# Kernel tuning notes

Measured on AMD Instinct MI355X. Metric: run time of the kernel, lower is better.

The kernel has to match this reference:

```python
import jax, jax.numpy as jnp
import numpy as np

DIM, H, KV, HD = 2048, 32, 8, 64
NREP = H // KV
EPS = 1e-6
NEG = -1e30


def _rope(x, cos, sin):
    # x: [B,S,h,HD], cos/sin: [S,HD//2]
    xr, xi = x[..., 0::2], x[..., 1::2]
    c = cos[None, :, None, :]
    s = sin[None, :, None, :]
    out = jnp.stack([xr * c - xi * s, xr * s + xi * c], axis=-1)
    return out.reshape(x.shape)


def _rmsnorm(x, w):
    xf = x.astype(jnp.float32)
    inv = jax.lax.rsqrt(jnp.mean(xf * xf, axis=-1, keepdims=True) + EPS)
    return (xf * inv * w).astype(x.dtype)


def setup_inputs() -> dict:
    key = jax.random.key(0)
    ks = jax.random.split(key, 9)
    B, S = 1, 2048
    x = jax.random.normal(ks[0], (B, S, DIM), jnp.float32)
    cos = jax.random.uniform(ks[1], (S, HD // 2), jnp.float32)
    sin = jax.random.uniform(ks[2], (S, HD // 2), jnp.float32)
    sc = 1.0 / np.sqrt(DIM)
    wq = jax.random.normal(ks[3], (DIM, DIM), jnp.float32) * sc
    wk = jax.random.normal(ks[4], (KV * HD, DIM), jnp.float32) * sc
    wv = jax.random.normal(ks[5], (KV * HD, DIM), jnp.float32) * sc
    wo = jax.random.normal(ks[6], (DIM, DIM), jnp.float32) * sc
    wg = jax.random.normal(ks[7], (DIM, DIM), jnp.float32) * sc
    qn = jnp.ones((HD,), jnp.float32)
    kn = jnp.ones((HD,), jnp.float32)
    return {"x": x, "cos": cos, "sin": sin, "wq": wq, "wk": wk, "wv": wv,
            "wo": wo, "wg": wg, "qn": qn, "kn": kn}


def reference(x, cos, sin, wq, wk, wv, wo, wg, qn, kn):
    B, S, _ = x.shape
    q = (x @ wq.T).reshape(B, S, H, HD)
    k = (x @ wk.T).reshape(B, S, KV, HD)
    v = (x @ wv.T).reshape(B, S, KV, HD)
    q = _rope(q, cos, sin)
    k = _rope(k, cos, sin)
    q = _rmsnorm(q, qn)
    k = _rmsnorm(k, kn)
    # GQA without materializing repeat_kv: head h = g*NREP + r uses kv head g
    qg = q.reshape(B, S, KV, NREP, HD)
    scale = 1.0 / np.sqrt(HD)
    scores = jnp.einsum('bqgrd,bkgd->bgrqk', qg, k) * scale  # [B,KV,NREP,S,S]
    causal = jnp.tril(jnp.ones((S, S), bool))
    scores = jnp.where(causal, scores, NEG)
    attn = jax.nn.softmax(scores, axis=-1)
    o = jnp.einsum('bgrqk,bkgd->bqgrd', attn, v).reshape(B, S, DIM)
    o = o * jax.nn.sigmoid(x @ wg.T)
    return o @ wo.T
```

## Files before the change

kernel.cpp:

```cpp
#include <hip/hip_runtime.h>
#include <stdint.h>

typedef unsigned short u16;
typedef __bf16 bf16x8 __attribute__((ext_vector_type(8)));
typedef float f32x4 __attribute__((ext_vector_type(4)));

__device__ __forceinline__ float bf2f(u16 u) {
  union { unsigned int i; float f; } v; v.i = ((unsigned int)u) << 16; return v.f;
}
__device__ __forceinline__ u16 f2bf(float f) {
  union { float f; unsigned int i; } v; v.f = f;
  unsigned int r = v.i + 0x7fffu + ((v.i >> 16) & 1u);
  return (u16)(r >> 16);
}
__device__ __forceinline__ u16 f2bf_trunc(float f) {
  union { float f; unsigned int i; } v; v.f = f;
  return (u16)(v.i >> 16);
}
__device__ __forceinline__ void ld16(const void* g, void* l) {
  __builtin_amdgcn_global_load_lds(
      (const __attribute__((address_space(1))) unsigned int*)g,
      (__attribute__((address_space(3))) unsigned int*)l, 16, 0, 0);
}

__global__ __launch_bounds__(256) void k_cast(
    const float* __restrict__ s0, u16* __restrict__ d0,
    const float* __restrict__ s1, u16* __restrict__ d1,
    const float* __restrict__ s2, u16* __restrict__ d2,
    const float* __restrict__ s3, u16* __restrict__ d3,
    const float* __restrict__ s4, u16* __restrict__ d4,
    const float* __restrict__ s5, u16* __restrict__ d5)
{
  int b = blockIdx.x;
  const float* s; u16* d;
  if (b < 4096)       { s = s0; d = d0; }
  else if (b < 8192)  { s = s1; d = d1; b -= 4096; }
  else if (b < 9216)  { s = s2; d = d2; b -= 8192; }
  else if (b < 10240) { s = s3; d = d3; b -= 9216; }
  else if (b < 14336) { s = s4; d = d4; b -= 10240; }
  else                { s = s5; d = d5; b -= 14336; }
  const int i = (b * 256 + threadIdx.x) * 4;
  const float4 v = *(const float4*)(s + i);
  ushort4 o;
  o.x = f2bf(v.x); o.y = f2bf(v.y); o.z = f2bf(v.z); o.w = f2bf(v.w);
  *(ushort4*)(d + i) = o;
}

template <typename OT>
__device__ __forceinline__ void gemm_body(
    const u16* __restrict__ A, int lda,
    const u16* __restrict__ B, int ldb,
    OT* __restrict__ C, int ldc, int K,
    u16* As, u16* Bs)
{
  const int tid = threadIdx.x;
  const int wave = tid >> 6, lane = tid & 63;
  const int wrow = (wave >> 1) * 64, wcol = (wave & 1) * 64;
  const int fr = lane & 15, kg = lane >> 4;
  const int srl = lane >> 3;
  const int scg = (lane & 7) ^ srl;

  f32x4 acc[4][4];
  const f32x4 z = {0.f, 0.f, 0.f, 0.f};
  for (int i = 0; i < 4; i++) for (int j = 0; j < 4; j++) acc[i][j] = z;

  const u16* Ag = A + (size_t)(wave * 8 + srl) * lda + scg * 8;
  const u16* Bg = B + (size_t)(wave * 8 + srl) * ldb + scg * 8;
  u16* Asw = As + wave * 8 * 64;
  u16* Bsw = Bs + wave * 8 * 64;
  const int sxr = fr & 7;

  for (int k0 = 0; k0 < K; k0 += 64) {
    for (int i = 0; i < 4; i++) {
      ld16(Ag + k0 + (size_t)(i * 32) * lda, Asw + i * 32 * 64);
      ld16(Bg + k0 + (size_t)(i * 32) * ldb, Bsw + i * 32 * 64);
    }
    __syncthreads();
    bf16x8 af[4][2], bfr[4][2];
    for (int i = 0; i < 4; i++)
      for (int h = 0; h < 2; h++) {
        af[i][h]  = *(const bf16x8*)&As[(wrow + i * 16 + fr) * 64 + (((h * 4 + kg) ^ sxr)) * 8];
        bfr[i][h] = *(const bf16x8*)&Bs[(wcol + i * 16 + fr) * 64 + (((h * 4 + kg) ^ sxr)) * 8];
      }
    for (int h = 0; h < 2; h++)
      for (int mi = 0; mi < 4; mi++)
        for (int ni = 0; ni < 4; ni++)
          acc[mi][ni] = __builtin_amdgcn_mfma_f32_16x16x32_bf16(af[mi][h], bfr[ni][h], acc[mi][ni], 0, 0, 0);
    __syncthreads();
  }
  const int er = kg * 4, ec = fr;
  for (int mi = 0; mi < 4; mi++)
    for (int ni = 0; ni < 4; ni++)
      for (int r = 0; r < 4; r++) {
        const float v = acc[mi][ni][r];
        OT* p = C + (size_t)(wrow + mi * 16 + er + r) * ldc + wcol + ni * 16 + ec;
        if constexpr (sizeof(OT) == 2) *p = (OT)f2bf(v); else *p = (OT)v;
      }
}

__global__ __launch_bounds__(256) void k_gemm_qkvg(
    const u16* __restrict__ x, const u16* __restrict__ wq, const u16* __restrict__ wk,
    const u16* __restrict__ wv, const u16* __restrict__ wg, u16* __restrict__ out)
{
  __shared__ __align__(16) u16 As[128 * 64];
  __shared__ __align__(16) u16 Bs[128 * 64];
  const int m0 = blockIdx.x * 128;
  const int c0 = blockIdx.y * 128;
  const u16* B; int br;
  if (c0 < 2048)      { B = wq; br = c0; }
  else if (c0 < 2560) { B = wk; br = c0 - 2048; }
  else if (c0 < 3072) { B = wv; br = c0 - 2560; }
  else                { B = wg; br = c0 - 3072; }
  gemm_body<u16>(x + (size_t)m0 * 2048, 2048, B + (size_t)br * 2048, 2048,
                 out + (size_t)m0 * 5120 + c0, 5120, 2048, As, Bs);
}

__global__ __launch_bounds__(256) void k_gemm_out(
    const u16* __restrict__ a, const u16* __restrict__ wo, float* __restrict__ out)
{
  __shared__ __align__(16) u16 As[128 * 64];
  __shared__ __align__(16) u16 Bs[128 * 64];
  const int m0 = blockIdx.x * 128;
  const int c0 = blockIdx.y * 128;
  gemm_body<float>(a + (size_t)m0 * 2048, 2048, wo + (size_t)c0 * 2048, 2048,
                   out + (size_t)m0 * 2048 + c0, 2048, 2048, As, Bs);
}

__global__ __launch_bounds__(256) void k_prep(
    u16* __restrict__ qkvg, const float* __restrict__ cosp, const float* __restrict__ sinp,
    const float* __restrict__ qn, const float* __restrict__ kn, u16* __restrict__ vt)
{
  __shared__ u16 Ls[64 * 72];
  if (blockIdx.x < 10240) {
    const int wid = (blockIdx.x * 256 + threadIdx.x) >> 6;
    const int lane = threadIdx.x & 63;
    const int s = wid / 20, hp = wid - s * 20;
    const int h = hp * 2 + (lane >> 5);
    const int j = lane & 31;
    u16* base; const float* wn;
    if (h < 32) { base = qkvg + (size_t)s * 5120 + h * 64;                wn = qn; }
    else        { base = qkvg + (size_t)s * 5120 + 2048 + (h - 32) * 64; wn = kn; }
    const unsigned int u = *(const unsigned int*)(base + 2 * j);
    const float xr = bf2f((u16)(u & 0xffffu)), xi = bf2f((u16)(u >> 16));
    const float c = cosp[s * 32 + j], sn = sinp[s * 32 + j];
    const float o0 = xr * c - xi * sn;
    const float o1 = xr * sn + xi * c;
    float ss = o0 * o0 + o1 * o1;
    for (int m = 1; m <= 16; m <<= 1) ss += __shfl_xor(ss, m, 64);
    const float inv = rsqrtf(ss * (1.0f / 64.0f) + 1e-6f);
    const u16 r0 = f2bf(o0 * inv * wn[2 * j]);
    const u16 r1 = f2bf(o1 * inv * wn[2 * j + 1]);
    *(unsigned int*)(base + 2 * j) = (unsigned int)r0 | ((unsigned int)r1 << 16);
  } else {
    const int bb = blockIdx.x - 10240;
    const int s0 = (bb & 31) * 64, g0 = (bb >> 5) * 64;
    const int tid = threadIdx.x;
    const int lr = tid >> 4, lc = (tid & 15) * 4;
    for (int p = 0; p < 4; p++) {
      const int r = p * 16 + lr;
      *(ushort4*)&Ls[r * 72 + lc] = *(const ushort4*)&qkvg[(size_t)(s0 + r) * 5120 + 2560 + g0 + lc];
    }
    __syncthreads();
    for (int p = 0; p < 4; p++) {
      const int r = p * 16 + lr;
      ushort4 o;
      o.x = Ls[(lc + 0) * 72 + r];
      o.y = Ls[(lc + 1) * 72 + r];
      o.z = Ls[(lc + 2) * 72 + r];
      o.w = Ls[(lc + 3) * 72 + r];
      *(ushort4*)&vt[(size_t)(g0 + r) * 2048 + s0 + lc] = o;
    }
  }
}

__global__ __launch_bounds__(256) void k_attn_part(
    const u16* __restrict__ qkvg, const u16* __restrict__ vt,
    u16* __restrict__ part, float* __restrict__ ml)
{
  __shared__ __align__(16) u16 Ks[128 * 64];
  __shared__ __align__(16) u16 Vs[64 * 128];
  __shared__ __align__(16) u16 Ps[64 * 132];
  const int c = blockIdx.x, h = blockIdx.y, g = h >> 2;
  int qt, ci;
  if (c < 8)       { qt = c;                 ci = 0; }
  else if (c < 24) { qt = 8 + ((c - 8) >> 1);  ci = (c - 8) & 1; }
  else if (c < 48) { qt = 16 + (c - 24) / 3;   ci = (c - 24) % 3; }
  else             { qt = 24 + ((c - 48) >> 2); ci = (c - 48) & 3; }
  const int kb0 = ci * 512;
  const int kend = min(kb0 + 512, (qt + 1) * 64);
  const int q0 = qt * 64;
  const int tid = threadIdx.x, wave = tid >> 6, lane = tid & 63;
  const int fr = lane & 15, kg = lane >> 4, fq = kg * 8;
  const int sx = fr & 7;

  {
    const u16* Qg = qkvg + (size_t)(q0 + wave * 16 + (lane >> 3)) * 5120 + h * 64 + (lane & 7) * 8;
    ld16(Qg, Ks + wave * 1024);
    ld16(Qg + (size_t)8 * 5120, Ks + wave * 1024 + 512);
  }
  __syncthreads();
  const bf16x8 aq0 = *(const bf16x8*)&Ks[(wave * 16 + fr) * 64 + fq];
  const bf16x8 aq1 = *(const bf16x8*)&Ks[(wave * 16 + fr) * 64 + 32 + fq];
  __syncthreads();

  f32x4 o[4];
  const f32x4 z = {0.f, 0.f, 0.f, 0.f};
  for (int i = 0; i < 4; i++) o[i] = z;
  float lsum[4] = {0.f, 0.f, 0.f, 0.f};
  const int qrow = q0 + wave * 16 + kg * 4;

  const int krl = wave * 8 + (lane >> 3);
  const int kcg = (lane & 7) ^ (krl & 7);
  const int vrl = wave * 4 + kg;
  const int vcg = fr ^ (vrl & 7);

  for (int kb = kb0; kb < kend; kb += 128) {
    {
      const u16* Kg = qkvg + (size_t)(kb + krl) * 5120 + 2048 + g * 64 + kcg * 8;
      for (int i = 0; i < 4; i++)
        ld16(Kg + (size_t)(i * 32) * 5120, Ks + (i * 32 + wave * 8) * 64);
    }
    {
      const u16* Vg = vt + (size_t)(g * 64 + vrl) * 2048 + kb + vcg * 8;
      for (int i = 0; i < 4; i++)
        ld16(Vg + (size_t)(i * 16) * 2048, Vs + (i * 16 + wave * 4) * 128);
    }
    __syncthreads();

    f32x4 sc[8];
    for (int i = 0; i < 8; i++) sc[i] = z;
    for (int ni = 0; ni < 8; ni++) {
      const bf16x8 bk0 = *(const bf16x8*)&Ks[(ni * 16 + fr) * 64 + (kg ^ sx) * 8];
      const bf16x8 bk1 = *(const bf16x8*)&Ks[(ni * 16 + fr) * 64 + ((kg + 4) ^ sx) * 8];
      sc[ni] = __builtin_amdgcn_mfma_f32_16x16x32_bf16(aq0, bk0, sc[ni], 0, 0, 0);
      sc[ni] = __builtin_amdgcn_mfma_f32_16x16x32_bf16(aq1, bk1, sc[ni], 0, 0, 0);
    }

    for (int r = 0; r < 4; r++) {
      float ls = 0.f;
      for (int ni = 0; ni < 8; ni++) {
        const int key = kb + ni * 16 + fr;
        float p = __expf(fmaf(sc[ni][r], 0.125f, -8.0f));
        p = (key <= qrow + r) ? p : 0.f;
        ls += p;
        Ps[(wave * 16 + kg * 4 + r) * 132 + ni * 16 + fr] = f2bf_trunc(p);
      }
      lsum[r] += ls;
    }

    for (int k0 = 0; k0 < 128; k0 += 32) {
      const bf16x8 ap = *(const bf16x8*)&Ps[(wave * 16 + fr) * 132 + k0 + fq];
      for (int ni = 0; ni < 4; ni++) {
        const bf16x8 bv = *(const bf16x8*)&Vs[(ni * 16 + fr) * 128 + (((k0 >> 3) + kg) ^ sx) * 8];
        o[ni] = __builtin_amdgcn_mfma_f32_16x16x32_bf16(ap, bv, o[ni], 0, 0, 0);
      }
    }
    __syncthreads();
  }

  const int pbase = (h * 80 + c) * 4096;
  for (int r = 0; r < 4; r++) {
    float L = lsum[r];
    for (int m = 1; m <= 8; m <<= 1) L += __shfl_xor(L, m, 64);
    const int rl = wave * 16 + kg * 4 + r;
    for (int ni = 0; ni < 4; ni++)
      part[pbase + rl * 64 + ni * 16 + fr] = f2bf(o[ni][r]);
    if (fr == 0) ml[(h * 80 + c) * 64 + rl] = L;
  }
}

__global__ __launch_bounds__(256) void k_attn_comb(
    const u16* __restrict__ part, const float* __restrict__ ml,
    const u16* __restrict__ qkvg, u16* __restrict__ aout)
{
  const int qt = blockIdx.x, h = blockIdx.y;
  const int w = threadIdx.x >> 6, lane = threadIdx.x & 63;
  int cb, nch;
  if (qt < 8)       { cb = qt;               nch = 1; }
  else if (qt < 16) { cb = 8 + 2 * (qt - 8);  nch = 2; }
  else if (qt < 24) { cb = 24 + 3 * (qt - 16); nch = 3; }
  else              { cb = 48 + 4 * (qt - 24); nch = 4; }
  for (int r = 0; r < 16; r++) {
    const int rl = w * 16 + r;
    const int row = qt * 64 + rl;
    float L = 0.f, o = 0.f;
    for (int cc = 0; cc < nch; cc++) {
      L += ml[(h * 80 + cb + cc) * 64 + rl];
      o += bf2f(part[(h * 80 + cb + cc) * 4096 + rl * 64 + lane]);
    }
    const float gv = bf2f(qkvg[(size_t)row * 5120 + 3072 + h * 64 + lane]);
    const float sig = 1.0f / (1.0f + __expf(-gv));
    aout[(size_t)row * 2048 + h * 64 + lane] = f2bf(o / L * sig);
  }
}

extern "C" void kernel_launch(void* const* d_in, const int* in_sizes, int n_in,
                              void* d_out, int out_size, void* d_ws, size_t ws_size,
                              hipStream_t stream)
{
  const float* x  = (const float*)d_in[0];
  const float* cs = (const float*)d_in[1];
  const float* sn = (const float*)d_in[2];
  const float* wq = (const float*)d_in[3];
  const float* wk = (const float*)d_in[4];
  const float* wv = (const float*)d_in[5];
  const float* wo = (const float*)d_in[6];
  const float* wg = (const float*)d_in[7];
  const float* qn = (const float*)d_in[8];
  const float* kn = (const float*)d_in[9];
  float* out = (float*)d_out;

  u16* xb   = (u16*)d_ws;
  u16* wqb  = xb  + (size_t)4194304;
  u16* wkb  = wqb + (size_t)4194304;
  u16* wvb  = wkb + (size_t)1048576;
  u16* wgb  = wvb + (size_t)1048576;
  u16* wob  = wgb + (size_t)4194304;
  u16* qkvg = wob + (size_t)4194304;
  u16* vt   = qkvg + (size_t)2048 * 5120;
  u16* aws  = vt   + (size_t)512 * 2048;

  u16*   part = xb;
  float* ml   = (float*)(xb + (size_t)32 * 80 * 4096);

  k_cast<<<dim3(18432), 256, 0, stream>>>(x, xb, wq, wqb, wk, wkb, wv, wvb, wo, wob, wg, wgb);
  k_gemm_qkvg<<<dim3(16, 40), 256, 0, stream>>>(xb, wqb, wkb, wvb, wgb, qkvg);
  k_prep<<<dim3(10240 + 256), 256, 0, stream>>>(qkvg, cs, sn, qn, kn, vt);
  k_attn_part<<<dim3(80, 32), 256, 0, stream>>>(qkvg, vt, part, ml);
  k_attn_comb<<<dim3(32, 32), 256, 0, stream>>>(part, ml, qkvg, aws);
  k_gemm_out<<<dim3(16, 16), 256, 0, stream>>>(aws, wob, out);
}
```

Baseline: 295.4 us.

## Transpose QK MFMA output, alias P buffer onto K LDS, skip mask on full tiles

The score MFMA now takes its operands in swapped order, so each lane holds four consecutive keys for a single query row. That lets the softmax probabilities be packed as bf16 pairs and written into a swizzled P buffer that reuses the K shared memory, with a barrier added before the reuse. Causal masking is skipped for tiles lying entirely below the diagonal, exp is computed with exp2 using prescaled constants, and the row-sum reduction shrinks to two shuffles. Wave priority is raised around the MFMA loops. The goals are less LDS use (better occupancy), fewer bank conflicts and less per-element work, at the cost of an extra __syncthreads per tile.

Result: no change. 291.5 us (-1.3%).

```diff
diff --git a/kernel.cpp b/kernel.cpp
--- a/kernel.cpp
+++ b/kernel.cpp
@@ -2,7 +2,9 @@
 #include <stdint.h>
 
 typedef unsigned short u16;
+typedef unsigned int u32;
 typedef __bf16 bf16x8 __attribute__((ext_vector_type(8)));
+typedef __bf16 bf16x2 __attribute__((ext_vector_type(2)));
 typedef float f32x4 __attribute__((ext_vector_type(4)));
 
 __device__ __forceinline__ float bf2f(u16 u) {
@@ -12,10 +14,6 @@
   union { float f; unsigned int i; } v; v.f = f;
   unsigned int r = v.i + 0x7fffu + ((v.i >> 16) & 1u);
   return (u16)(r >> 16);
-}
-__device__ __forceinline__ u16 f2bf_trunc(float f) {
-  union { float f; unsigned int i; } v; v.f = f;
-  return (u16)(v.i >> 16);
 }
 __device__ __forceinline__ void ld16(const void* g, void* l) {
   __builtin_amdgcn_global_load_lds(
@@ -179,7 +177,7 @@
 {
   __shared__ __align__(16) u16 Ks[128 * 64];
   __shared__ __align__(16) u16 Vs[64 * 128];
-  __shared__ __align__(16) u16 Ps[64 * 132];
+  u16* Ps = Ks;
   const int c = blockIdx.x, h = blockIdx.y, g = h >> 2;
   int qt, ci;
   if (c < 8)       { qt = c;                 ci = 0; }
@@ -206,8 +204,9 @@
   f32x4 o[4];
   const f32x4 z = {0.f, 0.f, 0.f, 0.f};
   for (int i = 0; i < 4; i++) o[i] = z;
-  float lsum[4] = {0.f, 0.f, 0.f, 0.f};
-  const int qrow = q0 + wave * 16 + kg * 4;
+  float L = 0.f;
+  const int qrow = q0 + wave * 16 + fr;
+  const int prow = wave * 16 + fr;
 
   const int krl = wave * 8 + (lane >> 3);
   const int kcg = (lane & 7) ^ (krl & 7);
@@ -229,44 +228,72 @@
 
     f32x4 sc[8];
     for (int i = 0; i < 8; i++) sc[i] = z;
+    __builtin_amdgcn_s_setprio(1);
     for (int ni = 0; ni < 8; ni++) {
-      const bf16x8 bk0 = *(const bf16x8*)&Ks[(ni * 16 + fr) * 64 + (kg ^ sx) * 8];
-      const bf16x8 bk1 = *(const bf16x8*)&Ks[(ni * 16 + fr) * 64 + ((kg + 4) ^ sx) * 8];
-      sc[ni] = __builtin_amdgcn_mfma_f32_16x16x32_bf16(aq0, bk0, sc[ni], 0, 0, 0);
-      sc[ni] = __builtin_amdgcn_mfma_f32_16x16x32_bf16(aq1, bk1, sc[ni], 0, 0, 0);
-    }
-
-    for (int r = 0; r < 4; r++) {
-      float ls = 0.f;
+      const bf16x8 bk0 = *(const bf16x8*)&Ks[(ni * 16 + fr) * 64 + ((kg ^ sx)) * 8];
+      const bf16x8 bk1 = *(const bf16x8*)&Ks[(ni * 16 + fr) * 64 + (((kg + 4) ^ sx)) * 8];
+      sc[ni] = __builtin_amdgcn_mfma_f32_16x16x32_bf16(bk0, aq0, sc[ni], 0, 0, 0);
+      sc[ni] = __builtin_amdgcn_mfma_f32_16x16x32_bf16(bk1, aq1, sc[ni], 0, 0, 0);
+    }
+    __builtin_amdgcn_s_setprio(0);
+    __syncthreads();
+
+    u32* Ps32 = (u32*)Ps;
+    const int pb32 = prow * 64;
+    if (kb + 127 > q0 + wave * 16) {
       for (int ni = 0; ni < 8; ni++) {
-        const int key = kb + ni * 16 + fr;
-        float p = __expf(fmaf(sc[ni][r], 0.125f, -8.0f));
-        p = (key <= qrow + r) ? p : 0.f;
-        ls += p;
-        Ps[(wave * 16 + kg * 4 + r) * 132 + ni * 16 + fr] = f2bf_trunc(p);
-      }
-      lsum[r] += ls;
-    }
-
+        const int dlim = qrow - (kb + ni * 16 + kg * 4);
+        float p0 = exp2f(fmaf(sc[ni][0], 0.18033688f, -11.5415603f));
+        float p1 = exp2f(fmaf(sc[ni][1], 0.18033688f, -11.5415603f));
+        float p2 = exp2f(fmaf(sc[ni][2], 0.18033688f, -11.5415603f));
+        float p3 = exp2f(fmaf(sc[ni][3], 0.18033688f, -11.5415603f));
+        p0 = (0 <= dlim) ? p0 : 0.f;
+        p1 = (1 <= dlim) ? p1 : 0.f;
+        p2 = (2 <= dlim) ? p2 : 0.f;
+        p3 = (3 <= dlim) ? p3 : 0.f;
+        L += (p0 + p1) + (p2 + p3);
+        bf16x2 w0, w1;
+        w0[0] = (__bf16)p0; w0[1] = (__bf16)p1;
+        w1[0] = (__bf16)p2; w1[1] = (__bf16)p3;
+        const int a = pb32 + ((2 * ni + (kg >> 1)) ^ sx) * 4 + (kg & 1) * 2;
+        *(bf16x2*)&Ps32[a]     = w0;
+        *(bf16x2*)&Ps32[a + 1] = w1;
+      }
+    } else {
+      for (int ni = 0; ni < 8; ni++) {
+        float p0 = exp2f(fmaf(sc[ni][0], 0.18033688f, -11.5415603f));
+        float p1 = exp2f(fmaf(sc[ni][1], 0.18033688f, -11.5415603f));
+        float p2 = exp2f(fmaf(sc[ni][2], 0.18033688f, -11.5415603f));
+        float p3 = exp2f(fmaf(sc[ni][3], 0.18033688f, -11.5415603f));
+        L += (p0 + p1) + (p2 + p3);
+        bf16x2 w0, w1;
+        w0[0] = (__bf16)p0; w0[1] = (__bf16)p1;
+        w1[0] = (__bf16)p2; w1[1] = (__bf16)p3;
+        const int a = pb32 + ((2 * ni + (kg >> 1)) ^ sx) * 4 + (kg & 1) * 2;
+        *(bf16x2*)&Ps32[a]     = w0;
+        *(bf16x2*)&Ps32[a + 1] = w1;
+      }
+    }
+
+    __builtin_amdgcn_s_setprio(1);
     for (int k0 = 0; k0 < 128; k0 += 32) {
-      const bf16x8 ap = *(const bf16x8*)&Ps[(wave * 16 + fr) * 132 + k0 + fq];
+      const bf16x8 ap = *(const bf16x8*)&Ps[prow * 128 + ((((k0 >> 3) + kg)) ^ sx) * 8];
       for (int ni = 0; ni < 4; ni++) {
         const bf16x8 bv = *(const bf16x8*)&Vs[(ni * 16 + fr) * 128 + (((k0 >> 3) + kg) ^ sx) * 8];
         o[ni] = __builtin_amdgcn_mfma_f32_16x16x32_bf16(ap, bv, o[ni], 0, 0, 0);
       }
     }
-    __syncthreads();
-  }
-
+    __builtin_amdgcn_s_setprio(0);
+    __syncthreads();
+  }
+
+  L += __shfl_xor(L, 16, 64);
+  L += __shfl_xor(L, 32, 64);
   const int pbase = (h * 80 + c) * 4096;
-  for (int r = 0; r < 4; r++) {
-    float L = lsum[r];
-    for (int m = 1; m <= 8; m <<= 1) L += __shfl_xor(L, m, 64);
-    const int rl = wave * 16 + kg * 4 + r;
-    for (int ni = 0; ni < 4; ni++)
-      part[pbase + rl * 64 + ni * 16 + fr] = f2bf(o[ni][r]);
-    if (fr == 0) ml[(h * 80 + c) * 64 + rl] = L;
-  }
+  for (int ni = 0; ni < 4; ni++)
+    for (int r = 0; r < 4; r++)
+      part[pbase + (wave * 16 + kg * 4 + r) * 64 + ni * 16 + fr] = f2bf(o[ni][r]);
+  if (lane < 16) ml[(h * 80 + c) * 64 + wave * 16 + fr] = L;
 }
 
 __global__ __launch_bounds__(256) void k_attn_comb(
```
